# Performance work log

Hardware: AMD Instinct MI355X
Metric: run time of the kernel (lower is better)

The kernel has to match this reference:

```python
import jax, jax.numpy as jnp
import numpy as np

DIM = 256
DH = 64            # dim_head
HEADS = DIM // DH  # 4
WH = WW = 8        # window size
EPS = 1e-5


def setup_inputs() -> dict:
    key = jax.random.key(0)
    k1, k2, k3 = jax.random.split(key, 3)
    x = jax.random.normal(k1, (4, DIM, 256, 256), dtype=jnp.float32)
    Wqkv = jax.random.normal(k2, (3 * DIM, DIM), dtype=jnp.float32) * (DIM ** -0.5)
    Wout = jax.random.normal(k3, (DIM, DIM), dtype=jnp.float32) * (DIM ** -0.5)
    gamma = jnp.ones((DIM,), dtype=jnp.float32)
    beta = jnp.zeros((DIM,), dtype=jnp.float32)
    return {"x": x, "gamma": gamma, "beta": beta, "Wqkv": Wqkv, "Wout": Wout}


def _to_windows(t, B, nh, nw):
    # (B, nh*WH, nw*WW, HEADS*DH) -> (B, nh, nw, HEADS, WH*WW, DH)
    t = t.reshape(B, nh, WH, nw, WW, HEADS, DH)
    t = t.transpose(0, 1, 3, 5, 2, 4, 6)
    return t.reshape(B, nh, nw, HEADS, WH * WW, DH)


def reference(x, gamma, beta, Wqkv, Wout):
    B, C, H, W = x.shape
    residual = x
    xh = x.transpose(0, 2, 3, 1)  # (B, H, W, C)
    # LayerNorm over channel dim
    mu = jnp.mean(xh, axis=-1, keepdims=True)
    var = jnp.mean(jnp.square(xh - mu), axis=-1, keepdims=True)
    xn = (xh - mu) * jax.lax.rsqrt(var + EPS) * gamma + beta
    nh, nw = H // WH, W // WW
    qkv = jnp.einsum('bhwc,fc->bhwf', xn, Wqkv)  # (B,H,W,3C)
    q, k, v = jnp.split(qkv, 3, axis=-1)
    q = _to_windows(q, B, nh, nw)
    k = _to_windows(k, B, nh, nw)
    v = _to_windows(v, B, nh, nw)
    scale = DH ** -0.5
    scores = jnp.einsum('bnmhqd,bnmhkd->bnmhqk', q, k) * scale  # 64x64 per window
    attn = jax.nn.softmax(scores, axis=-1)
    o = jnp.einsum('bnmhqk,bnmhkd->bnmhqd', attn, v)
    # merge windows back: (B,nh,nw,HEADS,WH*WW,DH) -> (B,H,W,C)
    o = o.reshape(B, nh, nw, HEADS, WH, WW, DH)
    o = o.transpose(0, 1, 4, 2, 5, 3, 6).reshape(B, H, W, C)
    o = jnp.einsum('bhwc,fc->bhwf', o, Wout)
    return o.transpose(0, 3, 1, 2) + residual
```

## Files before the change

### kernel.cpp

```cpp
#include <hip/hip_runtime.h>

typedef __attribute__((ext_vector_type(8))) short short8;
typedef __attribute__((ext_vector_type(4))) float floatx4;
typedef __attribute__((ext_vector_type(2))) float floatx2;
typedef __attribute__((ext_vector_type(4))) unsigned short ushort4v;

#define DEVI static __device__ __forceinline__

DEVI unsigned short f2bf(float f) {
  unsigned int u = __float_as_uint(f);
  u = (u + 0x7fffu + ((u >> 16) & 1u)) >> 16;
  return (unsigned short)u;
}
DEVI float bf2f(unsigned short h) { return __uint_as_float(((unsigned int)h) << 16); }

DEVI int ridx2(int c, int t) { return c * 128 + (t ^ ((c & 7) << 3)); }
DEVI int xnaddr(int row, int chunk) { return row * 256 + (((chunk) ^ (row & 7)) << 3); }

DEVI short8 wpfrag(const unsigned short* __restrict__ wbf, int rb, int kc, int lane) {
  return *(const short8*)&wbf[(((size_t)rb * 8 + kc) * 64 + lane) * 8];
}

__global__ void wconv(const float* __restrict__ wqkv, const float* __restrict__ wout,
                      unsigned short* __restrict__ wbf) {
  int cl = blockIdx.x * 256 + threadIdx.x;
  int lane = cl & 63;
  int rbkc = cl >> 6;
  int kc = rbkc & 7;
  int rb = rbkc >> 3;
  int g = lane >> 4, l15 = lane & 15;
  const float* src = (rb < 48) ? wqkv : wout;
  int row = (rb < 48) ? rb * 16 + l15 : (rb - 48) * 16 + l15;
#pragma unroll
  for (int h = 0; h < 2; ++h)
#pragma unroll
    for (int e = 0; e < 4; ++e)
      wbf[(size_t)cl * 8 + h * 4 + e] = f2bf(src[row * 256 + kc * 32 + h * 16 + g * 4 + e]);
}

__global__ __launch_bounds__(512, 2) void k1a_qkv(
    const float* __restrict__ x, const float* __restrict__ gamma,
    const float* __restrict__ beta, const unsigned short* __restrict__ wbf,
    unsigned short* __restrict__ frag) {
  __shared__ __align__(16) unsigned short sx[128 * 256];
  __shared__ floatx2 psum[4][128];

  const int tid = threadIdx.x;
  const int lane = tid & 63;
  const int wv = tid >> 6;
  const int g = lane >> 4;
  const int l15 = lane & 15;

  const int id = ((blockIdx.x & 7) << 8) + (blockIdx.x >> 3);
  const int b = id >> 9;
  const int wy = (id >> 4) & 31;
  const int wxp = id & 15;
  const size_t xbase = ((size_t)b << 24) + (size_t)(wy * 8) * 256 + (size_t)(wxp * 16);

#pragma unroll
  for (int it = 0; it < 16; ++it) {
    int s = it * 512 + tid;
    int c = s >> 5, i = (s >> 2) & 7, j4 = s & 3;
    floatx4 v = *(const floatx4*)(x + xbase + (size_t)c * 65536 + i * 256 + j4 * 4);
    ushort4v u;
    u.x = f2bf(v.x); u.y = f2bf(v.y); u.z = f2bf(v.z); u.w = f2bf(v.w);
    *(ushort4v*)&sx[ridx2(c, i * 16 + j4 * 4)] = u;
  }
  __syncthreads();

  const int t = tid & 127;
  const int q = tid >> 7;
  unsigned int xr[32];
  float s1 = 0.f, s2 = 0.f;
#pragma unroll
  for (int cc = 0; cc < 32; ++cc) {
    unsigned int u0 = sx[ridx2(q * 64 + 2 * cc, t)];
    unsigned int u1 = sx[ridx2(q * 64 + 2 * cc + 1, t)];
    xr[cc] = u0 | (u1 << 16);
    float a = __uint_as_float(u0 << 16);
    float c2 = __uint_as_float(u1 << 16);
    s1 += a + c2;
    s2 = fmaf(a, a, s2); s2 = fmaf(c2, c2, s2);
  }
  { floatx2 p; p.x = s1; p.y = s2; psum[q][t] = p; }
  __syncthreads();

  float S1 = 0.f, S2 = 0.f;
#pragma unroll
  for (int p = 0; p < 4; ++p) { floatx2 pp = psum[p][t]; S1 += pp.x; S2 += pp.y; }
  const float mu = S1 * (1.f / 256.f);
  const float rstd = rsqrtf(S2 * (1.f / 256.f) - mu * mu + 1e-5f);

#pragma unroll
  for (int kk = 0; kk < 2; ++kk) {
    int kc = q * 2 + kk;
#pragma unroll
    for (int gc = 0; gc < 4; ++gc) {
      short8 s8;
#pragma unroll
      for (int hf = 0; hf < 2; ++hf)
#pragma unroll
        for (int e = 0; e < 4; ++e) {
          int lc = kk * 32 + hf * 16 + gc * 4 + e;
          int c = q * 64 + lc;
          unsigned int u = xr[lc >> 1];
          float xv = __uint_as_float((lc & 1) ? (u & 0xffff0000u) : (u << 16));
          float val = (xv - mu) * rstd * gamma[c] + beta[c];
          s8[hf * 4 + e] = (short)f2bf(val);
        }
      *(short8*)&sx[xnaddr(t, kc * 4 + gc)] = s8;
    }
  }
  __syncthreads();

  auto ldsfrag = [&](int row, int kc) -> short8 {
    return *(const short8*)&sx[xnaddr(row, kc * 4 + g)];
  };

  const int head = wv >> 1;
  const int win = wv & 1;
  auto srow = [&](int tl) { return (((tl) >> 3) << 4) + win * 8 + ((tl) & 7); };

  unsigned short* fr = frag + ((size_t)(id * 8 + wv) * 24) * 512 + (size_t)lane * 8;

#pragma unroll
  for (int qk = 0; qk < 2; ++qk) {
    floatx4 acc[4][4] = {};
    const int rbq = qk * 16 + head * 4;
#pragma unroll
    for (int kh = 0; kh < 2; ++kh) {
      short8 wreg[4][4];
#pragma unroll
      for (int kk = 0; kk < 4; ++kk)
#pragma unroll
        for (int mt = 0; mt < 4; ++mt)
          wreg[kk][mt] = wpfrag(wbf, rbq + mt, kh * 4 + kk, lane);
#pragma unroll
      for (int kk = 0; kk < 4; ++kk) {
        int kc = kh * 4 + kk;
        short8 Bv[4];
#pragma unroll
        for (int nt = 0; nt < 4; ++nt) Bv[nt] = ldsfrag(srow(nt * 16 + l15), kc);
#pragma unroll
        for (int mt = 0; mt < 4; ++mt)
#pragma unroll
          for (int nt = 0; nt < 4; ++nt)
            acc[mt][nt] = __builtin_amdgcn_mfma_f32_16x16x32_bf16(wreg[kk][mt], Bv[nt], acc[mt][nt], 0, 0, 0);
      }
    }
#pragma unroll
    for (int nt = 0; nt < 4; ++nt)
#pragma unroll
      for (int ks = 0; ks < 2; ++ks) {
        short8 f;
#pragma unroll
        for (int e = 0; e < 4; ++e) {
          f[e]     = (short)f2bf(acc[2 * ks][nt][e]);
          f[4 + e] = (short)f2bf(acc[2 * ks + 1][nt][e]);
        }
        *(short8*)&fr[(size_t)(qk * 8 + nt * 2 + ks) * 512] = f;
      }
  }

  {
    floatx4 acc[4][4] = {};
#pragma unroll
    for (int kh = 0; kh < 2; ++kh) {
      short8 wreg[4][4];
#pragma unroll
      for (int kk = 0; kk < 4; ++kk)
#pragma unroll
        for (int nt = 0; nt < 4; ++nt)
          wreg[kk][nt] = wpfrag(wbf, 32 + head * 4 + nt, kh * 4 + kk, lane);
#pragma unroll
      for (int kk = 0; kk < 4; ++kk) {
        int kc = kh * 4 + kk;
        short8 Av[4];
#pragma unroll
        for (int mt = 0; mt < 4; ++mt) Av[mt] = ldsfrag(srow(mt * 16 + l15), kc);
#pragma unroll
        for (int mt = 0; mt < 4; ++mt)
#pragma unroll
          for (int nt = 0; nt < 4; ++nt)
            acc[mt][nt] = __builtin_amdgcn_mfma_f32_16x16x32_bf16(Av[mt], wreg[kk][nt], acc[mt][nt], 0, 0, 0);
      }
    }
#pragma unroll
    for (int nt = 0; nt < 4; ++nt)
#pragma unroll
      for (int ks = 0; ks < 2; ++ks) {
        short8 f;
#pragma unroll
        for (int e = 0; e < 4; ++e) {
          f[e]     = (short)f2bf(acc[2 * ks][nt][e]);
          f[4 + e] = (short)f2bf(acc[2 * ks + 1][nt][e]);
        }
        *(short8*)&fr[(size_t)(16 + nt * 2 + ks) * 512] = f;
      }
  }
}

__global__ __launch_bounds__(256, 1) void k1b_attn(
    const unsigned short* __restrict__ frag, unsigned short* __restrict__ o_scr) {
  const int tid = threadIdx.x;
  const int lane = tid & 63;
  const int head = tid >> 6;
  const int g = lane >> 4;
  const int l15 = lane & 15;

  const int id = ((blockIdx.x & 7) << 8) + (blockIdx.x >> 3);
  const int b = id >> 9;
  const int wy = (id >> 4) & 31;
  const int wxp = id & 15;

  const float CEXP = 0.125f * 1.44269504088896f;

#pragma unroll 1
  for (int win = 0; win < 2; ++win) {
    const unsigned short* fr =
        frag + ((size_t)(id * 8 + head * 2 + win) * 24) * 512 + (size_t)lane * 8;

    short8 qkf[2][4][2];
#pragma unroll
    for (int qk = 0; qk < 2; ++qk)
#pragma unroll
      for (int nt = 0; nt < 4; ++nt)
#pragma unroll
        for (int ks = 0; ks < 2; ++ks)
          qkf[qk][nt][ks] = *(const short8*)&fr[(size_t)(qk * 8 + nt * 2 + ks) * 512];

    short8 pf[4][2];
#pragma unroll
    for (int nts = 0; nts < 4; ++nts) {
      floatx4 sac[4] = {};
#pragma unroll
      for (int ks = 0; ks < 2; ++ks)
#pragma unroll
        for (int mts = 0; mts < 4; ++mts)
          sac[mts] = __builtin_amdgcn_mfma_f32_16x16x32_bf16(qkf[1][mts][ks], qkf[0][nts][ks], sac[mts], 0, 0, 0);

      float m = sac[0][0];
#pragma unroll
      for (int mts = 0; mts < 4; ++mts)
#pragma unroll
        for (int r = 0; r < 4; ++r) m = fmaxf(m, sac[mts][r]);
      m = fmaxf(m, __shfl_xor(m, 16));
      m = fmaxf(m, __shfl_xor(m, 32));
      float sum = 0.f;
#pragma unroll
      for (int mts = 0; mts < 4; ++mts)
#pragma unroll
        for (int r = 0; r < 4; ++r) {
          float p = __builtin_amdgcn_exp2f((sac[mts][r] - m) * CEXP);
          sac[mts][r] = p;
          sum += p;
        }
      sum += __shfl_xor(sum, 16);
      sum += __shfl_xor(sum, 32);
      float inv = __builtin_amdgcn_rcpf(sum);
#pragma unroll
      for (int ks = 0; ks < 2; ++ks) {
        short8 f;
#pragma unroll
        for (int e = 0; e < 4; ++e) {
          f[e]     = (short)f2bf(sac[2 * ks][e] * inv);
          f[4 + e] = (short)f2bf(sac[2 * ks + 1][e] * inv);
        }
        pf[nts][ks] = f;
      }
    }

    short8 vf[4][2];
#pragma unroll
    for (int nt = 0; nt < 4; ++nt)
#pragma unroll
      for (int ks = 0; ks < 2; ++ks)
        vf[nt][ks] = *(const short8*)&fr[(size_t)(16 + nt * 2 + ks) * 512];

    floatx4 oa2[4][4];
#pragma unroll
    for (int dt = 0; dt < 4; ++dt)
#pragma unroll
      for (int ntq = 0; ntq < 4; ++ntq) oa2[dt][ntq] = floatx4{0.f, 0.f, 0.f, 0.f};
#pragma unroll
    for (int ks = 0; ks < 2; ++ks)
#pragma unroll
      for (int dt = 0; dt < 4; ++dt)
#pragma unroll
        for (int ntq = 0; ntq < 4; ++ntq)
          oa2[dt][ntq] = __builtin_amdgcn_mfma_f32_16x16x32_bf16(vf[dt][ks], pf[ntq][ks], oa2[dt][ntq], 0, 0, 0);

#pragma unroll
    for (int dtp = 0; dtp < 2; ++dtp)
#pragma unroll
      for (int ntq = 0; ntq < 4; ++ntq) {
        int tq = ntq * 16 + l15;
        size_t orow = ((size_t)b * 256 + wy * 8 + (tq >> 3)) * 256 + wxp * 16 + win * 8 + (tq & 7);
        short8 o8;
#pragma unroll
        for (int r = 0; r < 4; ++r) {
          o8[r]     = (short)f2bf(oa2[2 * dtp][ntq][r]);
          o8[4 + r] = (short)f2bf(oa2[2 * dtp + 1][ntq][r]);
        }
        *(short8*)&o_scr[orow * 256 + head * 64 + dtp * 32 + g * 8] = o8;
      }
  }
}

__global__ __launch_bounds__(512, 2) void k2_proj(
    const unsigned short* __restrict__ o_scr, const float* __restrict__ x,
    const unsigned short* __restrict__ wbf, float* __restrict__ out) {
  __shared__ __align__(16) unsigned short sx[128 * 256];

  const int tid = threadIdx.x;
  const int lane = tid & 63;
  const int wv = tid >> 6;
  const int g = lane >> 4;
  const int l15 = lane & 15;

  const int b = blockIdx.x >> 8;
  const int h = blockIdx.x & 255;

  auto ldsfrag = [&](int row, int kc) -> short8 {
    return *(const short8*)&sx[xnaddr(row, kc * 4 + g)];
  };

#pragma unroll
  for (int hf = 0; hf < 2; ++hf) {
    const size_t obase = (((size_t)b * 256 + h) * 256 + hf * 128) * 256;
#pragma unroll
    for (int it = 0; it < 8; ++it) {
      int s = it * 512 + tid;
      int tl = s >> 5, cid = s & 31;
      short8 v = *(const short8*)&o_scr[obase + tl * 256 + cid * 8];
      *(short8*)&sx[tl * 256 + ((cid ^ (tl & 7)) << 3)] = v;
    }
    __syncthreads();

    floatx4 fa[8][2] = {};
#pragma unroll
    for (int kc = 0; kc < 8; ++kc) {
      short8 Atok[8], Bw[2];
#pragma unroll
      for (int nt = 0; nt < 8; ++nt) Atok[nt] = ldsfrag(nt * 16 + l15, kc);
#pragma unroll
      for (int mt = 0; mt < 2; ++mt)
        Bw[mt] = wpfrag(wbf, 48 + wv * 2 + mt, kc, lane);
#pragma unroll
      for (int nt = 0; nt < 8; ++nt)
#pragma unroll
        for (int mt = 0; mt < 2; ++mt)
          fa[nt][mt] = __builtin_amdgcn_mfma_f32_16x16x32_bf16(Atok[nt], Bw[mt], fa[nt][mt], 0, 0, 0);
    }

#pragma unroll
    for (int nt = 0; nt < 8; ++nt)
#pragma unroll
      for (int mt = 0; mt < 2; ++mt) {
        int co = wv * 32 + mt * 16 + l15;
        size_t addr = (((size_t)(b * 256 + co)) << 16) + (size_t)h * 256 +
                      hf * 128 + nt * 16 + 4 * g;
        floatx4 xv = *(const floatx4*)(x + addr);
        floatx4 o;
#pragma unroll
        for (int r = 0; r < 4; ++r) o[r] = fa[nt][mt][r] + xv[r];
        *(floatx4*)(out + addr) = o;
      }
    __syncthreads();
  }
}

__global__ __launch_bounds__(512, 2) void fused_fallback(
    const float* __restrict__ x, const float* __restrict__ gamma,
    const float* __restrict__ beta, const unsigned short* __restrict__ wbf,
    float* __restrict__ out) {
  __shared__ __align__(16) unsigned short sres[256 * 128];
  __shared__ __align__(16) unsigned short sxn[128 * 256];

  const int tid = threadIdx.x;
  const int lane = tid & 63;
  const int wv = tid >> 6;
  const int g = lane >> 4;
  const int l15 = lane & 15;

  const int id = ((blockIdx.x & 7) << 8) + (blockIdx.x >> 3);
  const int b = id >> 9;
  const int wy = (id >> 4) & 31;
  const int wxp = id & 15;
  const size_t xbase = ((size_t)b << 24) + (size_t)(wy * 8) * 256 + (size_t)(wxp * 16);

#pragma unroll
  for (int it = 0; it < 16; ++it) {
    int s = it * 512 + tid;
    int c = s >> 5, i = (s >> 2) & 7, j4 = s & 3;
    floatx4 v = *(const floatx4*)(x + xbase + (size_t)c * 65536 + i * 256 + j4 * 4);
    ushort4v u;
    u.x = f2bf(v.x); u.y = f2bf(v.y); u.z = f2bf(v.z); u.w = f2bf(v.w);
    *(ushort4v*)&sres[ridx2(c, i * 16 + j4 * 4)] = u;
  }
  __syncthreads();

  const int t = tid & 127;
  const int q = tid >> 7;
  float s1 = 0.f, s2 = 0.f;
#pragma unroll 8
  for (int cc = 0; cc < 64; ++cc) {
    float xv = bf2f(sres[ridx2(q * 64 + cc, t)]);
    s1 += xv; s2 += xv * xv;
  }
  { floatx2 p; p.x = s1; p.y = s2; ((floatx2*)sxn)[q * 128 + t] = p; }
  __syncthreads();

  float S1 = 0.f, S2 = 0.f;
#pragma unroll
  for (int p = 0; p < 4; ++p) {
    floatx2 pp = ((const floatx2*)sxn)[p * 128 + t];
    S1 += pp.x; S2 += pp.y;
  }
  const float mu = S1 * (1.f / 256.f);
  const float rstd = rsqrtf(S2 * (1.f / 256.f) - mu * mu + 1e-5f);
  __syncthreads();

#pragma unroll
  for (int kk = 0; kk < 2; ++kk) {
    int kc = q * 2 + kk;
#pragma unroll
    for (int gc = 0; gc < 4; ++gc) {
      short8 s8;
#pragma unroll
      for (int hf = 0; hf < 2; ++hf)
#pragma unroll
        for (int e = 0; e < 4; ++e) {
          int c = kc * 32 + hf * 16 + gc * 4 + e;
          float xv = bf2f(sres[ridx2(c, t)]);
          float val = (xv - mu) * rstd * gamma[c] + beta[c];
          s8[hf * 4 + e] = (short)f2bf(val);
        }
      *(short8*)&sxn[xnaddr(t, kc * 4 + gc)] = s8;
    }
  }
  __syncthreads();

  auto ldsfrag = [&](int row, int kc) -> short8 {
    return *(const short8*)&sxn[xnaddr(row, kc * 4 + g)];
  };

  const int head = wv >> 1;
  const int win = wv & 1;
  auto srow = [&](int tl) { return (((tl) >> 3) << 4) + win * 8 + ((tl) & 7); };

  short8 qkf[2][4][2];
#pragma unroll
  for (int qk = 0; qk < 2; ++qk) {
    floatx4 acc[4][4] = {};
    const int rbq = qk * 16 + head * 4;
#pragma unroll
    for (int kc = 0; kc < 8; ++kc) {
      short8 Bv[4], Av[4];
#pragma unroll
      for (int nt = 0; nt < 4; ++nt) Bv[nt] = ldsfrag(srow(nt * 16 + l15), kc);
#pragma unroll
      for (int mt = 0; mt < 4; ++mt)
        Av[mt] = wpfrag(wbf, rbq + mt, kc, lane);
#pragma unroll
      for (int mt = 0; mt < 4; ++mt)
#pragma unroll
        for (int nt = 0; nt < 4; ++nt)
          acc[mt][nt] = __builtin_amdgcn_mfma_f32_16x16x32_bf16(Av[mt], Bv[nt], acc[mt][nt], 0, 0, 0);
    }
#pragma unroll
    for (int nt = 0; nt < 4; ++nt)
#pragma unroll
      for (int ks = 0; ks < 2; ++ks) {
        short8 f;
#pragma unroll
        for (int e = 0; e < 4; ++e) {
          f[e]     = (short)f2bf(acc[2 * ks][nt][e]);
          f[4 + e] = (short)f2bf(acc[2 * ks + 1][nt][e]);
        }
        qkf[qk][nt][ks] = f;
      }
  }

  floatx4 sa[4][4] = {};
#pragma unroll
  for (int ks = 0; ks < 2; ++ks)
#pragma unroll
    for (int mts = 0; mts < 4; ++mts)
#pragma unroll
      for (int nts = 0; nts < 4; ++nts)
        sa[mts][nts] = __builtin_amdgcn_mfma_f32_16x16x32_bf16(qkf[1][mts][ks], qkf[0][nts][ks], sa[mts][nts], 0, 0, 0);

  short8 pf[4][2];
  const float CEXP = 0.125f * 1.44269504088896f;
#pragma unroll
  for (int nts = 0; nts < 4; ++nts) {
    float m = sa[0][nts][0];
#pragma unroll
    for (int mts = 0; mts < 4; ++mts)
#pragma unroll
      for (int r = 0; r < 4; ++r) m = fmaxf(m, sa[mts][nts][r]);
    m = fmaxf(m, __shfl_xor(m, 16));
    m = fmaxf(m, __shfl_xor(m, 32));
    float sum = 0.f;
#pragma unroll
    for (int mts = 0; mts < 4; ++mts)
#pragma unroll
      for (int r = 0; r < 4; ++r) {
        float p = __builtin_amdgcn_exp2f((sa[mts][nts][r] - m) * CEXP);
        sa[mts][nts][r] = p;
        sum += p;
      }
    sum += __shfl_xor(sum, 16);
    sum += __shfl_xor(sum, 32);
    float inv = __builtin_amdgcn_rcpf(sum);
#pragma unroll
    for (int ks = 0; ks < 2; ++ks) {
      short8 f;
#pragma unroll
      for (int e = 0; e < 4; ++e) {
        f[e]     = (short)f2bf(sa[2 * ks][nts][e] * inv);
        f[4 + e] = (short)f2bf(sa[2 * ks + 1][nts][e] * inv);
      }
      pf[nts][ks] = f;
    }
  }

  short8 vf[4][2];
  {
    floatx4 acc[4][4] = {};
#pragma unroll
    for (int kc = 0; kc < 8; ++kc) {
      short8 Av[4], Bv[4];
#pragma unroll
      for (int mt = 0; mt < 4; ++mt) Av[mt] = ldsfrag(srow(mt * 16 + l15), kc);
#pragma unroll
      for (int nt = 0; nt < 4; ++nt)
        Bv[nt] = wpfrag(wbf, 32 + head * 4 + nt, kc, lane);
#pragma unroll
      for (int mt = 0; mt < 4; ++mt)
#pragma unroll
        for (int nt = 0; nt < 4; ++nt)
          acc[mt][nt] = __builtin_amdgcn_mfma_f32_16x16x32_bf16(Av[mt], Bv[nt], acc[mt][nt], 0, 0, 0);
    }
#pragma unroll
    for (int nt = 0; nt < 4; ++nt)
#pragma unroll
      for (int ks = 0; ks < 2; ++ks) {
        short8 f;
#pragma unroll
        for (int e = 0; e < 4; ++e) {
          f[e]     = (short)f2bf(acc[2 * ks][nt][e]);
          f[4 + e] = (short)f2bf(acc[2 * ks + 1][nt][e]);
        }
        vf[nt][ks] = f;
      }
  }

  floatx4 oa[4][4] = {};
#pragma unroll
  for (int ks = 0; ks < 2; ++ks)
#pragma unroll
    for (int ntq = 0; ntq < 4; ++ntq)
#pragma unroll
      for (int dt = 0; dt < 4; ++dt)
        oa[ntq][dt] = __builtin_amdgcn_mfma_f32_16x16x32_bf16(pf[ntq][ks], vf[dt][ks], oa[ntq][dt], 0, 0, 0);

  __syncthreads();

#pragma unroll
  for (int ntq = 0; ntq < 4; ++ntq)
#pragma unroll
    for (int dt = 0; dt < 4; ++dt) {
      int c = head * 64 + dt * 16 + l15;
      int kc = c >> 5, hf = (c >> 4) & 1, gc = (c >> 2) & 3, e = c & 3;
#pragma unroll
      for (int r = 0; r < 4; ++r) {
        int tq = ntq * 16 + 4 * g + r;
        int sr = srow(tq);
        sxn[sr * 256 + (((kc * 4 + gc) ^ (sr & 7)) << 3) + hf * 4 + e] =
            f2bf(oa[ntq][dt][r]);
      }
    }
  __syncthreads();

  floatx4 fa[2][8] = {};
#pragma unroll
  for (int kc = 0; kc < 8; ++kc) {
    short8 Bv[8], Av[2];
#pragma unroll
    for (int nt = 0; nt < 8; ++nt) Bv[nt] = ldsfrag(nt * 16 + l15, kc);
#pragma unroll
    for (int mt = 0; mt < 2; ++mt)
      Av[mt] = wpfrag(wbf, 48 + wv * 2 + mt, kc, lane);
#pragma unroll
    for (int mt = 0; mt < 2; ++mt)
#pragma unroll
      for (int nt = 0; nt < 8; ++nt)
        fa[mt][nt] = __builtin_amdgcn_mfma_f32_16x16x32_bf16(Av[mt], Bv[nt], fa[mt][nt], 0, 0, 0);
  }

#pragma unroll
  for (int mt = 0; mt < 2; ++mt)
#pragma unroll
    for (int nt = 0; nt < 8; ++nt)
#pragma unroll
      for (int r = 0; r < 4; ++r) {
        int co = wv * 32 + mt * 16 + 4 * g + r;
        int tt = nt * 16 + l15;
        float val = fa[mt][nt][r] + bf2f(sres[ridx2(co, tt)]);
        out[((size_t)(b * 256 + co) << 16) + (size_t)(wy * 8 + (tt >> 4)) * 256 +
            (wxp * 16 + (tt & 15))] = val;
      }
}

extern "C" void kernel_launch(void* const* d_in, const int* in_sizes, int n_in,
                              void* d_out, int out_size, void* d_ws, size_t ws_size,
                              hipStream_t stream) {
  const float* x     = (const float*)d_in[0];
  const float* gamma = (const float*)d_in[1];
  const float* beta  = (const float*)d_in[2];
  const float* wqkv  = (const float*)d_in[3];
  const float* wout  = (const float*)d_in[4];
  float* out = (float*)d_out;

  unsigned short* wbf   = (unsigned short*)d_ws;
  unsigned short* o_scr = wbf + 262144;
  unsigned short* frag  = o_scr + 67108864;

  const size_t need = 512 * 1024 + (size_t)128 * 1024 * 1024 + (size_t)384 * 1024 * 1024;

  wconv<<<128, 256, 0, stream>>>(wqkv, wout, wbf);
  if (ws_size >= need) {
    k1a_qkv<<<2048, 512, 0, stream>>>(x, gamma, beta, wbf, frag);
    k1b_attn<<<2048, 256, 0, stream>>>(frag, o_scr);
    k2_proj<<<1024, 512, 0, stream>>>(o_scr, x, wbf, out);
  } else {
    fused_fallback<<<2048, 512, 0, stream>>>(x, gamma, beta, wbf, out);
  }
}
```

Baseline: 496.8 us.

## Move QKV projection into attention kernel, store normalized input instead of QKV

```diff
diff --git a/kernel.cpp b/kernel.cpp
--- a/kernel.cpp
+++ b/kernel.cpp
@@ -38,16 +38,14 @@
       wbf[(size_t)cl * 8 + h * 4 + e] = f2bf(src[row * 256 + kc * 32 + h * 16 + g * 4 + e]);
 }
 
-__global__ __launch_bounds__(512, 2) void k1a_qkv(
+__global__ __launch_bounds__(512, 2) void k0_ln(
     const float* __restrict__ x, const float* __restrict__ gamma,
-    const float* __restrict__ beta, const unsigned short* __restrict__ wbf,
-    unsigned short* __restrict__ frag) {
+    const float* __restrict__ beta, unsigned short* __restrict__ xng) {
   __shared__ __align__(16) unsigned short sx[128 * 256];
   __shared__ floatx2 psum[4][128];
 
   const int tid = threadIdx.x;
   const int lane = tid & 63;
-  const int wv = tid >> 6;
   const int g = lane >> 4;
   const int l15 = lane & 15;
 
@@ -113,95 +111,21 @@
   }
   __syncthreads();
 
-  auto ldsfrag = [&](int row, int kc) -> short8 {
-    return *(const short8*)&sx[xnaddr(row, kc * 4 + g)];
-  };
-
-  const int head = wv >> 1;
-  const int win = wv & 1;
-  auto srow = [&](int tl) { return (((tl) >> 3) << 4) + win * 8 + ((tl) & 7); };
-
-  unsigned short* fr = frag + ((size_t)(id * 8 + wv) * 24) * 512 + (size_t)lane * 8;
-
-#pragma unroll
-  for (int qk = 0; qk < 2; ++qk) {
-    floatx4 acc[4][4] = {};
-    const int rbq = qk * 16 + head * 4;
-#pragma unroll
-    for (int kh = 0; kh < 2; ++kh) {
-      short8 wreg[4][4];
-#pragma unroll
-      for (int kk = 0; kk < 4; ++kk)
-#pragma unroll
-        for (int mt = 0; mt < 4; ++mt)
-          wreg[kk][mt] = wpfrag(wbf, rbq + mt, kh * 4 + kk, lane);
-#pragma unroll
-      for (int kk = 0; kk < 4; ++kk) {
-        int kc = kh * 4 + kk;
-        short8 Bv[4];
-#pragma unroll
-        for (int nt = 0; nt < 4; ++nt) Bv[nt] = ldsfrag(srow(nt * 16 + l15), kc);
-#pragma unroll
-        for (int mt = 0; mt < 4; ++mt)
-#pragma unroll
-          for (int nt = 0; nt < 4; ++nt)
-            acc[mt][nt] = __builtin_amdgcn_mfma_f32_16x16x32_bf16(wreg[kk][mt], Bv[nt], acc[mt][nt], 0, 0, 0);
-      }
-    }
-#pragma unroll
-    for (int nt = 0; nt < 4; ++nt)
-#pragma unroll
-      for (int ks = 0; ks < 2; ++ks) {
-        short8 f;
-#pragma unroll
-        for (int e = 0; e < 4; ++e) {
-          f[e]     = (short)f2bf(acc[2 * ks][nt][e]);
-          f[4 + e] = (short)f2bf(acc[2 * ks + 1][nt][e]);
-        }
-        *(short8*)&fr[(size_t)(qk * 8 + nt * 2 + ks) * 512] = f;
-      }
-  }
-
-  {
-    floatx4 acc[4][4] = {};
-#pragma unroll
-    for (int kh = 0; kh < 2; ++kh) {
-      short8 wreg[4][4];
-#pragma unroll
-      for (int kk = 0; kk < 4; ++kk)
-#pragma unroll
-        for (int nt = 0; nt < 4; ++nt)
-          wreg[kk][nt] = wpfrag(wbf, 32 + head * 4 + nt, kh * 4 + kk, lane);
-#pragma unroll
-      for (int kk = 0; kk < 4; ++kk) {
-        int kc = kh * 4 + kk;
-        short8 Av[4];
-#pragma unroll
-        for (int mt = 0; mt < 4; ++mt) Av[mt] = ldsfrag(srow(mt * 16 + l15), kc);
-#pragma unroll
-        for (int mt = 0; mt < 4; ++mt)
-#pragma unroll
-          for (int nt = 0; nt < 4; ++nt)
-            acc[mt][nt] = __builtin_amdgcn_mfma_f32_16x16x32_bf16(Av[mt], wreg[kk][nt], acc[mt][nt], 0, 0, 0);
-      }
-    }
-#pragma unroll
-    for (int nt = 0; nt < 4; ++nt)
-#pragma unroll
-      for (int ks = 0; ks < 2; ++ks) {
-        short8 f;
-#pragma unroll
-        for (int e = 0; e < 4; ++e) {
-          f[e]     = (short)f2bf(acc[2 * ks][nt][e]);
-          f[4 + e] = (short)f2bf(acc[2 * ks + 1][nt][e]);
-        }
-        *(short8*)&fr[(size_t)(16 + nt * 2 + ks) * 512] = f;
-      }
-  }
-}
-
-__global__ __launch_bounds__(256, 1) void k1b_attn(
-    const unsigned short* __restrict__ frag, unsigned short* __restrict__ o_scr) {
+  const int wv = tid >> 6;
+#pragma unroll
+  for (int it = 0; it < 8; ++it) {
+    int ci = it * 8 + wv;
+    int win = ci >> 5, nt = (ci >> 3) & 3, kc = ci & 7;
+    int tq = nt * 16 + l15;
+    int tl = ((tq >> 3) << 4) + win * 8 + (tq & 7);
+    short8 v = *(const short8*)&sx[xnaddr(tl, kc * 4 + g)];
+    *(short8*)&xng[(((size_t)id * 64 + ci) * 64 + lane) * 8] = v;
+  }
+}
+
+__global__ __launch_bounds__(256, 1) void k1_qkv_attn(
+    const unsigned short* __restrict__ xng, const unsigned short* __restrict__ wbf,
+    unsigned short* __restrict__ o_scr) {
   const int tid = threadIdx.x;
   const int lane = tid & 63;
   const int head = tid >> 6;
@@ -215,19 +139,47 @@
 
   const float CEXP = 0.125f * 1.44269504088896f;
 
+  auto tfrag = [&](int win, int nt, int kc) -> short8 {
+    return *(const short8*)&xng[(((size_t)id * 64 + win * 32 + nt * 8 + kc) * 64 + lane) * 8];
+  };
+
 #pragma unroll 1
   for (int win = 0; win < 2; ++win) {
-    const unsigned short* fr =
-        frag + ((size_t)(id * 8 + head * 2 + win) * 24) * 512 + (size_t)lane * 8;
-
-    short8 qkf[2][4][2];
-#pragma unroll
-    for (int qk = 0; qk < 2; ++qk)
-#pragma unroll
-      for (int nt = 0; nt < 4; ++nt)
-#pragma unroll
-        for (int ks = 0; ks < 2; ++ks)
-          qkf[qk][nt][ks] = *(const short8*)&fr[(size_t)(qk * 8 + nt * 2 + ks) * 512];
+    floatx4 accQ[4][4] = {}, accK[4][4] = {};
+#pragma unroll
+    for (int kc = 0; kc < 8; ++kc) {
+      short8 tf[4], wq[4], wk[4];
+#pragma unroll
+      for (int nt = 0; nt < 4; ++nt) tf[nt] = tfrag(win, nt, kc);
+#pragma unroll
+      for (int mt = 0; mt < 4; ++mt) {
+        wq[mt] = wpfrag(wbf, head * 4 + mt, kc, lane);
+        wk[mt] = wpfrag(wbf, 16 + head * 4 + mt, kc, lane);
+      }
+#pragma unroll
+      for (int mt = 0; mt < 4; ++mt)
+#pragma unroll
+        for (int nt = 0; nt < 4; ++nt) {
+          accQ[mt][nt] = __builtin_amdgcn_mfma_f32_16x16x32_bf16(wq[mt], tf[nt], accQ[mt][nt], 0, 0, 0);
+          accK[mt][nt] = __builtin_amdgcn_mfma_f32_16x16x32_bf16(wk[mt], tf[nt], accK[mt][nt], 0, 0, 0);
+        }
+    }
+    short8 qf[4][2], kf[4][2];
+#pragma unroll
+    for (int nt = 0; nt < 4; ++nt)
+#pragma unroll
+      for (int ks = 0; ks < 2; ++ks) {
+        short8 fq, fk;
+#pragma unroll
+        for (int e = 0; e < 4; ++e) {
+          fq[e]     = (short)f2bf(accQ[2 * ks][nt][e]);
+          fq[4 + e] = (short)f2bf(accQ[2 * ks + 1][nt][e]);
+          fk[e]     = (short)f2bf(accK[2 * ks][nt][e]);
+          fk[4 + e] = (short)f2bf(accK[2 * ks + 1][nt][e]);
+        }
+        qf[nt][ks] = fq;
+        kf[nt][ks] = fk;
+      }
 
     short8 pf[4][2];
 #pragma unroll
@@ -237,7 +189,7 @@
       for (int ks = 0; ks < 2; ++ks)
 #pragma unroll
         for (int mts = 0; mts < 4; ++mts)
-          sac[mts] = __builtin_amdgcn_mfma_f32_16x16x32_bf16(qkf[1][mts][ks], qkf[0][nts][ks], sac[mts], 0, 0, 0);
+          sac[mts] = __builtin_amdgcn_mfma_f32_16x16x32_bf16(kf[mts][ks], qf[nts][ks], sac[mts], 0, 0, 0);
 
       float m = sac[0][0];
 #pragma unroll
@@ -271,11 +223,34 @@
     }
 
     short8 vf[4][2];
-#pragma unroll
-    for (int nt = 0; nt < 4; ++nt)
-#pragma unroll
-      for (int ks = 0; ks < 2; ++ks)
-        vf[nt][ks] = *(const short8*)&fr[(size_t)(16 + nt * 2 + ks) * 512];
+    {
+      floatx4 acc[4][4] = {};
+#pragma unroll
+      for (int kc = 0; kc < 8; ++kc) {
+        short8 tf[4], wv4[4];
+#pragma unroll
+        for (int mt = 0; mt < 4; ++mt) tf[mt] = tfrag(win, mt, kc);
+#pragma unroll
+        for (int nt = 0; nt < 4; ++nt) wv4[nt] = wpfrag(wbf, 32 + head * 4 + nt, kc, lane);
+#pragma unroll
+        for (int mt = 0; mt < 4; ++mt)
+#pragma unroll
+          for (int nt = 0; nt < 4; ++nt)
+            acc[mt][nt] = __builtin_amdgcn_mfma_f32_16x16x32_bf16(tf[mt], wv4[nt], acc[mt][nt], 0, 0, 0);
+      }
+#pragma unroll
+      for (int nt = 0; nt < 4; ++nt)
+#pragma unroll
+        for (int ks = 0; ks < 2; ++ks) {
+          short8 f;
+#pragma unroll
+          for (int e = 0; e < 4; ++e) {
+            f[e]     = (short)f2bf(acc[2 * ks][nt][e]);
+            f[4 + e] = (short)f2bf(acc[2 * ks + 1][nt][e]);
+          }
+          vf[nt][ks] = f;
+        }
+    }
 
     floatx4 oa2[4][4];
 #pragma unroll
@@ -626,14 +601,14 @@
 
   unsigned short* wbf   = (unsigned short*)d_ws;
   unsigned short* o_scr = wbf + 262144;
-  unsigned short* frag  = o_scr + 67108864;
-
-  const size_t need = 512 * 1024 + (size_t)128 * 1024 * 1024 + (size_t)384 * 1024 * 1024;
+  unsigned short* xng   = o_scr + 67108864;
+
+  const size_t need = 512 * 1024 + (size_t)256 * 1024 * 1024;
 
   wconv<<<128, 256, 0, stream>>>(wqkv, wout, wbf);
   if (ws_size >= need) {
-    k1a_qkv<<<2048, 512, 0, stream>>>(x, gamma, beta, wbf, frag);
-    k1b_attn<<<2048, 256, 0, stream>>>(frag, o_scr);
+    k0_ln<<<2048, 512, 0, stream>>>(x, gamma, beta, xng);
+    k1_qkv_attn<<<2048, 256, 0, stream>>>(xng, wbf, o_scr);
     k2_proj<<<1024, 512, 0, stream>>>(o_scr, x, wbf, out);
   } else {
     fused_fallback<<<2048, 512, 0, stream>>>(x, gamma, beta, wbf, out);
```

Result: slower. 662.8 us (+33.4%).
